# Optimization experiments

Measured on AMD Instinct MI355X. Metric: run time of the kernel, lower is better.

The kernel has to match this reference:

```python
import jax, jax.numpy as jnp
import numpy as np

N = 50000
E = 800000
IN_CH = 128
HID = 16
HEADS = 8
OUT_CH = 64
NEG_SLOPE = 0.2


def setup_inputs() -> dict:
    key = jax.random.key(0)
    ks = jax.random.split(key, 16)
    x = jax.random.normal(ks[0], (N, IN_CH), dtype=jnp.float32)
    edge_index = jax.random.randint(ks[1], (2, E), 0, N, dtype=jnp.int64)
    s = 0.05
    # GATv2 layer 1: in=128 -> heads=8, out=16 (concat -> 128)
    W1l = jax.random.normal(ks[2], (IN_CH, HEADS * HID), dtype=jnp.float32) * s
    b1l = jnp.zeros((HEADS * HID,), dtype=jnp.float32)
    W1r = jax.random.normal(ks[3], (IN_CH, HEADS * HID), dtype=jnp.float32) * s
    b1r = jnp.zeros((HEADS * HID,), dtype=jnp.float32)
    att1 = jax.random.normal(ks[4], (HEADS, HID), dtype=jnp.float32) * s
    bias1 = jnp.zeros((HEADS * HID,), dtype=jnp.float32)
    # GATv2 layer 2: in=128 -> heads=1, out=64
    W2l = jax.random.normal(ks[5], (HEADS * HID, OUT_CH), dtype=jnp.float32) * s
    b2l = jnp.zeros((OUT_CH,), dtype=jnp.float32)
    W2r = jax.random.normal(ks[6], (HEADS * HID, OUT_CH), dtype=jnp.float32) * s
    b2r = jnp.zeros((OUT_CH,), dtype=jnp.float32)
    att2 = jax.random.normal(ks[7], (1, OUT_CH), dtype=jnp.float32) * s
    bias2 = jnp.zeros((OUT_CH,), dtype=jnp.float32)
    return dict(x=x, edge_index=edge_index,
                W1l=W1l, b1l=b1l, W1r=W1r, b1r=b1r, att1=att1, bias1=bias1,
                W2l=W2l, b2l=b2l, W2r=W2r, b2r=b2r, att2=att2, bias2=bias2)


def gatv2_conv(x, src, dst, Wl, bl, Wr, br, att, bias, heads, out_ch, concat):
    n = x.shape[0]
    xl = (x @ Wl + bl).reshape(n, heads, out_ch)  # source transform
    xr = (x @ Wr + br).reshape(n, heads, out_ch)  # target transform
    m = xl[src] + xr[dst]                          # [E, H, C]
    m = jnp.where(m > 0, m, NEG_SLOPE * m)         # LeakyReLU(0.2)
    alpha = jnp.einsum('ehc,hc->eh', m, att)       # [E, H]
    # segment softmax over destination nodes (every node has a self loop)
    amax = jax.ops.segment_max(alpha, dst, num_segments=n)
    ea = jnp.exp(alpha - amax[dst])
    denom = jax.ops.segment_sum(ea, dst, num_segments=n)
    w = ea / denom[dst]                            # [E, H]
    out = jax.ops.segment_sum(xl[src] * w[:, :, None], dst, num_segments=n)
    if concat:
        out = out.reshape(n, heads * out_ch)
    else:
        out = out.mean(axis=1)
    return out + bias


def reference(x, edge_index, W1l, b1l, W1r, b1r, att1, bias1,
              W2l, b2l, W2r, b2r, att2, bias2):
    n = x.shape[0]
    loops = jnp.arange(n, dtype=edge_index.dtype)
    src = jnp.concatenate([edge_index[0], loops])
    dst = jnp.concatenate([edge_index[1], loops])
    # dropout layers are identity in eval mode
    h = gatv2_conv(x, src, dst, W1l, b1l, W1r, b1r, att1, bias1,
                   heads=HEADS, out_ch=HID, concat=True)
    h = jax.nn.elu(h)
    out = gatv2_conv(h, src, dst, W2l, b2l, W2r, b2r, att2, bias2,
                     heads=1, out_ch=OUT_CH, concat=True)
    return out
```

## Files before the change

kernel.cpp:

```cpp
#include <hip/hip_runtime.h>
#include <hip/hip_bf16.h>

constexpr int N_  = 50000;
constexpr int E_  = 800000;
constexpr int ET_ = 850000;
constexpr float NEG_SLOPE = 0.2f;

constexpr int SCAN_NB = (N_ + 255) / 256;
constexpr int CSR_CAP = 1250008;
constexpr int HT      = ET_ / 8;
constexpr int HB      = (HT + 255) / 256;
constexpr int G1A     = 1563;
constexpr int G1Bb    = 1562;
constexpr int ZERO4   = (50000 + CSR_CAP) / 4;

typedef __attribute__((ext_vector_type(8))) short short8;
typedef __attribute__((ext_vector_type(4))) float f32x4;

__device__ inline float leaky(float v) { return fmaxf(v, NEG_SLOPE * v); }

__device__ inline unsigned bf16rn(float f) {
    union { float f; unsigned u; } v; v.f = f;
    return (v.u + 0x7fffu + ((v.u >> 16) & 1u)) >> 16;
}
__device__ inline float2 unpack2(unsigned u) {
    return make_float2(__uint_as_float(u << 16), __uint_as_float(u & 0xffff0000u));
}

__global__ __launch_bounds__(256) void init_kernel(
        const float* __restrict__ W1l, const float* __restrict__ W1r,
        const float* __restrict__ W2l, const float* __restrict__ W2r,
        unsigned short* __restrict__ wsw, unsigned short* __restrict__ wsw2,
        int4* __restrict__ zbase) {
    int gid = blockIdx.x * 256 + threadIdx.x;
    if (gid < ZERO4) zbase[gid] = make_int4(0, 0, 0, 0);
    if (gid < 32768) {
        int j    = gid & 7;
        int lane = (gid >> 3) & 63;
        int ks   = (gid >> 9) & 3;
        int ct   = gid >> 11;
        int k = ks * 32 + ((lane >> 4) & 3) * 8 + j;
        int c = ct * 16 + (lane & 15);
        float v = (c < 128) ? W1l[k * 128 + c] : W1r[k * 128 + (c - 128)];
        wsw[gid] = (unsigned short)bf16rn(v);
    } else if (gid < 49152) {
        int t2   = gid - 32768;
        int j    = t2 & 7;
        int lane = (t2 >> 3) & 63;
        int ks   = (t2 >> 9) & 3;
        int ct   = t2 >> 11;
        int k = ks * 32 + ((lane >> 4) & 3) * 8 + j;
        int c = ct * 16 + (lane & 15);
        float v = (c < 64) ? W2l[k * 64 + c] : W2r[k * 64 + (c - 64)];
        wsw2[t2] = (unsigned short)bf16rn(v);
    }
}

__global__ __launch_bounds__(256) void scan_partial(
        const int* __restrict__ count, int* __restrict__ bsum) {
    __shared__ int red[256];
    int t = threadIdx.x;
    int i = blockIdx.x * 256 + t;
    red[t] = (i < N_) ? ((count[i] + 7) & ~7) : 0;
    __syncthreads();
    #pragma unroll
    for (int o = 128; o > 0; o >>= 1) {
        if (t < o) red[t] += red[t + o];
        __syncthreads();
    }
    if (t == 0) bsum[blockIdx.x] = red[0];
}

__global__ __launch_bounds__(256) void scan_final2(
        const int* __restrict__ count, const int* __restrict__ bsum,
        int* __restrict__ start, int* __restrict__ cur) {
    __shared__ int top[256];
    __shared__ int buf[256];
    int t = threadIdx.x;
    top[t] = (t < SCAN_NB) ? bsum[t] : 0;
    __syncthreads();
    #pragma unroll
    for (int o = 1; o < 256; o <<= 1) {
        int add = (t >= o) ? top[t - o] : 0;
        __syncthreads();
        top[t] += add;
        __syncthreads();
    }
    int bst = (blockIdx.x == 0) ? 0 : top[blockIdx.x - 1];
    int i = blockIdx.x * 256 + t;
    int v = (i < N_) ? ((count[i] + 7) & ~7) : 0;
    buf[t] = v;
    __syncthreads();
    #pragma unroll
    for (int o = 1; o < 256; o <<= 1) {
        int add = (t >= o) ? buf[t - o] : 0;
        __syncthreads();
        buf[t] += add;
        __syncthreads();
    }
    if (i < N_) {
        int sv = bst + buf[t] - v;
        start[i] = sv;
        cur[i]   = sv;
    }
}

__global__ __launch_bounds__(256) void edge_gemm1(
        const int phase, const int nbase,
        const int* __restrict__ ei, int* __restrict__ count,
        int* __restrict__ cur, int* __restrict__ csr_src,
        const float* __restrict__ x, const unsigned short* __restrict__ wsw,
        const float* __restrict__ bl, const float* __restrict__ br,
        unsigned short* __restrict__ xlu, float* __restrict__ xr1) {
    __shared__ unsigned short lu[16][132];
    __shared__ float          lr[16][132];
    if (blockIdx.x < HB) {
        int t = blockIdx.x * 256 + threadIdx.x;
        if (t >= HT) return;
        int e8 = t * 8;
        if (phase == 0) {
            int d[8];
            if (e8 < E_) {
                int4 a = *(const int4*)(ei + E_ + e8);
                int4 b = *(const int4*)(ei + E_ + e8 + 4);
                d[0] = a.x; d[1] = a.y; d[2] = a.z; d[3] = a.w;
                d[4] = b.x; d[5] = b.y; d[6] = b.z; d[7] = b.w;
            } else {
                #pragma unroll
                for (int i = 0; i < 8; ++i) d[i] = e8 + i - E_;
            }
            #pragma unroll
            for (int i = 0; i < 8; ++i) atomicAdd(&count[d[i]], 1);
        } else {
            int s[8], d[8];
            if (e8 < E_) {
                int4 sa = *(const int4*)(ei + e8);
                int4 sb = *(const int4*)(ei + e8 + 4);
                int4 da = *(const int4*)(ei + E_ + e8);
                int4 db = *(const int4*)(ei + E_ + e8 + 4);
                s[0] = sa.x; s[1] = sa.y; s[2] = sa.z; s[3] = sa.w;
                s[4] = sb.x; s[5] = sb.y; s[6] = sb.z; s[7] = sb.w;
                d[0] = da.x; d[1] = da.y; d[2] = da.z; d[3] = da.w;
                d[4] = db.x; d[5] = db.y; d[6] = db.z; d[7] = db.w;
            } else {
                #pragma unroll
                for (int i = 0; i < 8; ++i) { s[i] = e8 + i - E_; d[i] = s[i]; }
            }
            int o[8];
            #pragma unroll
            for (int i = 0; i < 8; ++i) o[i] = atomicAdd(&cur[d[i]], 1);
            #pragma unroll
            for (int i = 0; i < 8; ++i) csr_src[o[i]] = s[i];
        }
        return;
    }
    const int blk  = blockIdx.x - HB;
    const int wave = threadIdx.x >> 6;
    const int lane = threadIdx.x & 63;
    const int n0 = nbase + blk * 16;
    const int m = lane & 15;
    const int q = (lane >> 4) & 3;
    const float* __restrict__ arow = x + (size_t)(n0 + m) * 128 + q * 8;
    short8 afrag[4];
    #pragma unroll
    for (int ks = 0; ks < 4; ++ks) {
        float4 v0 = *(const float4*)(arow + ks * 32);
        float4 v1 = *(const float4*)(arow + ks * 32 + 4);
        short8 a;
        a[0] = (short)bf16rn(v0.x); a[1] = (short)bf16rn(v0.y);
        a[2] = (short)bf16rn(v0.z); a[3] = (short)bf16rn(v0.w);
        a[4] = (short)bf16rn(v1.x); a[5] = (short)bf16rn(v1.y);
        a[6] = (short)bf16rn(v1.z); a[7] = (short)bf16rn(v1.w);
        afrag[ks] = a;
    }
    #pragma unroll
    for (int i = 0; i < 4; ++i) {
        const int ct = wave * 4 + i;
        f32x4 acc = {0.f, 0.f, 0.f, 0.f};
        #pragma unroll
        for (int ks = 0; ks < 4; ++ks) {
            short8 b = *(const short8*)(wsw + ((size_t)(ct * 4 + ks) * 64 + lane) * 8);
            acc = __builtin_amdgcn_mfma_f32_16x16x32_bf16(afrag[ks], b, acc, 0, 0, 0);
        }
        if (ct < 8) {
            const int col = ct * 16 + m;
            float bias = bl[col];
            #pragma unroll
            for (int j = 0; j < 4; ++j)
                lu[q * 4 + j][col] = (unsigned short)bf16rn(acc[j] + bias);
        } else {
            const int col = (ct - 8) * 16 + m;
            float bias = br[col];
            #pragma unroll
            for (int j = 0; j < 4; ++j)
                lr[q * 4 + j][col] = acc[j] + bias;
        }
    }
    __syncthreads();
    unsigned* __restrict__ xlu32 = (unsigned*)xlu;
    #pragma unroll
    for (int k = 0; k < 4; ++k) {
        int r = wave * 4 + k;
        unsigned w = *(const unsigned*)&lu[r][2 * lane];
        xlu32[(size_t)(n0 + r) * 64 + lane] = w;
        float2 f = make_float2(lr[r][2 * lane], lr[r][2 * lane + 1]);
        *(float2*)(xr1 + (size_t)(n0 + r) * 128 + 2 * lane) = f;
    }
}

__global__ __launch_bounds__(256) void fused1(
        const int* __restrict__ csr_src, const int* __restrict__ start,
        const int* __restrict__ count,
        const unsigned* __restrict__ xl1b, const float* __restrict__ xr1,
        const float* __restrict__ att, const float* __restrict__ bias1,
        float* __restrict__ hout) {
    int t = blockIdx.x * 256 + threadIdx.x;
    int n = __builtin_amdgcn_readfirstlane(t >> 6);
    int lane = t & 63;
    if (n >= N_) return;
    float2 xr = *(const float2*)(xr1 + (size_t)n * 128 + 2 * lane);
    float2 av = *(const float2*)(att + 2 * lane);
    int p0 = __builtin_amdgcn_readfirstlane(start[n]);
    int p1 = p0 + __builtin_amdgcn_readfirstlane(count[n]);
    float2 acc = make_float2(0.f, 0.f);
    float l = 0.f;
    for (int p = p0; p < p1; p += 8) {
        int4 ia = *(const int4*)(csr_src + p);
        int4 ib = *(const int4*)(csr_src + p + 4);
        int s0 = __builtin_amdgcn_readfirstlane(ia.x);
        int s1 = __builtin_amdgcn_readfirstlane(ia.y);
        int s2 = __builtin_amdgcn_readfirstlane(ia.z);
        int s3 = __builtin_amdgcn_readfirstlane(ia.w);
        int s4 = __builtin_amdgcn_readfirstlane(ib.x);
        int s5 = __builtin_amdgcn_readfirstlane(ib.y);
        int s6 = __builtin_amdgcn_readfirstlane(ib.z);
        int s7 = __builtin_amdgcn_readfirstlane(ib.w);
        float2 x0 = unpack2(xl1b[(size_t)s0 * 64 + lane]);
        float2 x1 = unpack2(xl1b[(size_t)s1 * 64 + lane]);
        float2 x2 = unpack2(xl1b[(size_t)s2 * 64 + lane]);
        float2 x3 = unpack2(xl1b[(size_t)s3 * 64 + lane]);
        float2 x4 = unpack2(xl1b[(size_t)s4 * 64 + lane]);
        float2 x5 = unpack2(xl1b[(size_t)s5 * 64 + lane]);
        float2 x6 = unpack2(xl1b[(size_t)s6 * 64 + lane]);
        float2 x7 = unpack2(xl1b[(size_t)s7 * 64 + lane]);
        float a0 = fmaf(leaky(x0.x + xr.x), av.x, leaky(x0.y + xr.y) * av.y);
        float a1 = fmaf(leaky(x1.x + xr.x), av.x, leaky(x1.y + xr.y) * av.y);
        float a2 = fmaf(leaky(x2.x + xr.x), av.x, leaky(x2.y + xr.y) * av.y);
        float a3 = fmaf(leaky(x3.x + xr.x), av.x, leaky(x3.y + xr.y) * av.y);
        float a4 = fmaf(leaky(x4.x + xr.x), av.x, leaky(x4.y + xr.y) * av.y);
        float a5 = fmaf(leaky(x5.x + xr.x), av.x, leaky(x5.y + xr.y) * av.y);
        float a6 = fmaf(leaky(x6.x + xr.x), av.x, leaky(x6.y + xr.y) * av.y);
        float a7 = fmaf(leaky(x7.x + xr.x), av.x, leaky(x7.y + xr.y) * av.y);
        a0 += __shfl_xor(a0, 1); a1 += __shfl_xor(a1, 1);
        a2 += __shfl_xor(a2, 1); a3 += __shfl_xor(a3, 1);
        a4 += __shfl_xor(a4, 1); a5 += __shfl_xor(a5, 1);
        a6 += __shfl_xor(a6, 1); a7 += __shfl_xor(a7, 1);
        a0 += __shfl_xor(a0, 2); a1 += __shfl_xor(a1, 2);
        a2 += __shfl_xor(a2, 2); a3 += __shfl_xor(a3, 2);
        a4 += __shfl_xor(a4, 2); a5 += __shfl_xor(a5, 2);
        a6 += __shfl_xor(a6, 2); a7 += __shfl_xor(a7, 2);
        a0 += __shfl_xor(a0, 4); a1 += __shfl_xor(a1, 4);
        a2 += __shfl_xor(a2, 4); a3 += __shfl_xor(a3, 4);
        a4 += __shfl_xor(a4, 4); a5 += __shfl_xor(a5, 4);
        a6 += __shfl_xor(a6, 4); a7 += __shfl_xor(a7, 4);
        float w0 = __expf(a0);
        float w1 = p + 1 < p1 ? __expf(a1) : 0.f;
        float w2 = p + 2 < p1 ? __expf(a2) : 0.f;
        float w3 = p + 3 < p1 ? __expf(a3) : 0.f;
        float w4 = p + 4 < p1 ? __expf(a4) : 0.f;
        float w5 = p + 5 < p1 ? __expf(a5) : 0.f;
        float w6 = p + 6 < p1 ? __expf(a6) : 0.f;
        float w7 = p + 7 < p1 ? __expf(a7) : 0.f;
        acc.x = fmaf(w0, x0.x, acc.x); acc.y = fmaf(w0, x0.y, acc.y); l += w0;
        acc.x = fmaf(w1, x1.x, acc.x); acc.y = fmaf(w1, x1.y, acc.y); l += w1;
        acc.x = fmaf(w2, x2.x, acc.x); acc.y = fmaf(w2, x2.y, acc.y); l += w2;
        acc.x = fmaf(w3, x3.x, acc.x); acc.y = fmaf(w3, x3.y, acc.y); l += w3;
        acc.x = fmaf(w4, x4.x, acc.x); acc.y = fmaf(w4, x4.y, acc.y); l += w4;
        acc.x = fmaf(w5, x5.x, acc.x); acc.y = fmaf(w5, x5.y, acc.y); l += w5;
        acc.x = fmaf(w6, x6.x, acc.x); acc.y = fmaf(w6, x6.y, acc.y); l += w6;
        acc.x = fmaf(w7, x7.x, acc.x); acc.y = fmaf(w7, x7.y, acc.y); l += w7;
    }
    float2 bv = *(const float2*)(bias1 + 2 * lane);
    float vx = acc.x / l + bv.x;
    float vy = acc.y / l + bv.y;
    float2 o;
    o.x = vx > 0.f ? vx : (__expf(vx) - 1.f);
    o.y = vy > 0.f ? vy : (__expf(vy) - 1.f);
    *(float2*)(hout + (size_t)n * 128 + 2 * lane) = o;
}

__global__ __launch_bounds__(256) void gemm2_mfma(
        const float* __restrict__ hbuf,
        const unsigned short* __restrict__ wsw2,
        const float* __restrict__ bl, const float* __restrict__ br,
        unsigned short* __restrict__ xlu2, float* __restrict__ xr2) {
    __shared__ unsigned short lu2[16][68];
    __shared__ float          lr2[16][68];
    const int wave = threadIdx.x >> 6;
    const int lane = threadIdx.x & 63;
    const int n0 = blockIdx.x * 16;
    const int m = lane & 15;
    const int q = (lane >> 4) & 3;
    const float* __restrict__ arow = hbuf + (size_t)(n0 + m) * 128 + q * 8;
    short8 afrag[4];
    #pragma unroll
    for (int ks = 0; ks < 4; ++ks) {
        float4 v0 = *(const float4*)(arow + ks * 32);
        float4 v1 = *(const float4*)(arow + ks * 32 + 4);
        short8 a;
        a[0] = (short)bf16rn(v0.x); a[1] = (short)bf16rn(v0.y);
        a[2] = (short)bf16rn(v0.z); a[3] = (short)bf16rn(v0.w);
        a[4] = (short)bf16rn(v1.x); a[5] = (short)bf16rn(v1.y);
        a[6] = (short)bf16rn(v1.z); a[7] = (short)bf16rn(v1.w);
        afrag[ks] = a;
    }
    #pragma unroll
    for (int i = 0; i < 2; ++i) {
        const int ct = wave * 2 + i;
        f32x4 acc = {0.f, 0.f, 0.f, 0.f};
        #pragma unroll
        for (int ks = 0; ks < 4; ++ks) {
            short8 b = *(const short8*)(wsw2 + ((size_t)(ct * 4 + ks) * 64 + lane) * 8);
            acc = __builtin_amdgcn_mfma_f32_16x16x32_bf16(afrag[ks], b, acc, 0, 0, 0);
        }
        if (ct < 4) {
            const int col = ct * 16 + m;
            float bias = bl[col];
            #pragma unroll
            for (int j = 0; j < 4; ++j)
                lu2[q * 4 + j][col] = (unsigned short)bf16rn(acc[j] + bias);
        } else {
            const int col = (ct - 4) * 16 + m;
            float bias = br[col];
            #pragma unroll
            for (int j = 0; j < 4; ++j)
                lr2[q * 4 + j][col] = acc[j] + bias;
        }
    }
    __syncthreads();
    unsigned* __restrict__ xlu232 = (unsigned*)xlu2;
    #pragma unroll
    for (int k = 0; k < 2; ++k) {
        int rr = wave * 4 + 2 * k + (lane >> 5);
        int c  = lane & 31;
        unsigned w = *(const unsigned*)&lu2[rr][2 * c];
        xlu232[(size_t)(n0 + rr) * 32 + c] = w;
    }
    #pragma unroll
    for (int k = 0; k < 4; ++k) {
        int r = wave * 4 + k;
        xr2[(size_t)(n0 + r) * 64 + lane] = lr2[r][lane];
    }
}

__global__ __launch_bounds__(256) void fused2(
        const int* __restrict__ csr_src, const int* __restrict__ start,
        const int* __restrict__ count,
        const unsigned* __restrict__ xl2b, const float* __restrict__ xr2,
        const float* __restrict__ att, const float* __restrict__ bias2,
        float* __restrict__ out) {
    int t = blockIdx.x * 256 + threadIdx.x;
    int n = __builtin_amdgcn_readfirstlane(t >> 6);
    int lane = t & 63;
    int half = lane >> 5;
    int lc   = lane & 31;
    if (n >= N_) return;
    float2 xr = *(const float2*)(xr2 + (size_t)n * 64 + 2 * lc);
    float2 av = *(const float2*)(att + 2 * lc);
    int p0 = __builtin_amdgcn_readfirstlane(start[n]);
    int p1 = p0 + __builtin_amdgcn_readfirstlane(count[n]);
    float2 acc = make_float2(0.f, 0.f);
    float l = 0.f;
    for (int p = p0; p < p1; p += 8) {
        int4 ia = *(const int4*)(csr_src + p);
        int4 ib = *(const int4*)(csr_src + p + 4);
        int sx[8];
        sx[0] = __builtin_amdgcn_readfirstlane(ia.x);
        sx[1] = __builtin_amdgcn_readfirstlane(ia.y);
        sx[2] = __builtin_amdgcn_readfirstlane(ia.z);
        sx[3] = __builtin_amdgcn_readfirstlane(ia.w);
        sx[4] = __builtin_amdgcn_readfirstlane(ib.x);
        sx[5] = __builtin_amdgcn_readfirstlane(ib.y);
        sx[6] = __builtin_amdgcn_readfirstlane(ib.z);
        sx[7] = __builtin_amdgcn_readfirstlane(ib.w);
        #pragma unroll
        for (int u = 0; u < 4; ++u) {
            int pe = p + 2 * u + half;
            int s  = sx[2 * u + half];
            float2 xv = unpack2(xl2b[(size_t)s * 32 + lc]);
            float a = fmaf(leaky(xv.x + xr.x), av.x, leaky(xv.y + xr.y) * av.y);
            a += __shfl_xor(a, 1);
            a += __shfl_xor(a, 2);
            a += __shfl_xor(a, 4);
            a += __shfl_xor(a, 8);
            a += __shfl_xor(a, 16);
            float w = pe < p1 ? __expf(a) : 0.f;
            acc.x = fmaf(w, xv.x, acc.x);
            acc.y = fmaf(w, xv.y, acc.y);
            l += w;
        }
    }
    acc.x += __shfl_xor(acc.x, 32);
    acc.y += __shfl_xor(acc.y, 32);
    l     += __shfl_xor(l, 32);
    if (half == 0) {
        float2 bv = *(const float2*)(bias2 + 2 * lc);
        float2 o;
        o.x = acc.x / l + bv.x;
        o.y = acc.y / l + bv.y;
        *(float2*)(out + (size_t)n * 64 + 2 * lc) = o;
    }
}

extern "C" void kernel_launch(void* const* d_in, const int* in_sizes, int n_in,
                              void* d_out, int out_size, void* d_ws, size_t ws_size,
                              hipStream_t stream) {
    (void)in_sizes; (void)n_in; (void)out_size; (void)ws_size;
    const float* x     = (const float*)d_in[0];
    const int*   ei    = (const int*)d_in[1];
    const float* W1l   = (const float*)d_in[2];
    const float* b1l   = (const float*)d_in[3];
    const float* W1r   = (const float*)d_in[4];
    const float* b1r   = (const float*)d_in[5];
    const float* att1  = (const float*)d_in[6];
    const float* bias1 = (const float*)d_in[7];
    const float* W2l   = (const float*)d_in[8];
    const float* b2l   = (const float*)d_in[9];
    const float* W2r   = (const float*)d_in[10];
    const float* b2r   = (const float*)d_in[11];
    const float* att2  = (const float*)d_in[12];
    const float* bias2 = (const float*)d_in[13];
    float* out = (float*)d_out;

    float* xr1      = (float*)d_ws;
    float* hbuf     = xr1 + 6400000;
    unsigned* xl1b  = (unsigned*)(hbuf + 6400000);
    int* count   = (int*)(xl1b + 3200000);
    int* csr_src = count + 50000;
    int* startp  = csr_src + CSR_CAP;
    int* cur     = startp + 50000;
    int* bsum    = cur + 850000;
    int* bstart  = bsum + 256;
    unsigned short* wsw2 = (unsigned short*)(bstart + 256);
    unsigned* xl2b = xl1b;
    float* xr2     = xr1;
    unsigned short* wsw = (unsigned short*)hbuf;

    init_kernel<<<(ZERO4 + 255) / 256, 256, 0, stream>>>(W1l, W1r, W2l, W2r,
                                                         wsw, wsw2, (int4*)count);
    edge_gemm1<<<HB + G1A, 256, 0, stream>>>(0, 0, ei, count, cur, csr_src,
                                             x, wsw, b1l, b1r,
                                             (unsigned short*)xl1b, xr1);
    scan_partial<<<SCAN_NB, 256, 0, stream>>>(count, bsum);
    scan_final2 <<<SCAN_NB, 256, 0, stream>>>(count, bsum, startp, cur);
    edge_gemm1<<<HB + G1Bb, 256, 0, stream>>>(1, G1A * 16, ei, count, cur, csr_src,
                                              x, wsw, b1l, b1r,
                                              (unsigned short*)xl1b, xr1);
    fused1<<<(N_ * 64 + 255) / 256, 256, 0, stream>>>(csr_src, startp, count,
                                                      xl1b, xr1, att1, bias1, hbuf);
    gemm2_mfma <<<N_ / 16, 256, 0, stream>>>(hbuf, wsw2, b2l, b2r,
                                             (unsigned short*)xl2b, xr2);
    fused2<<<(N_ * 64 + 255) / 256, 256, 0, stream>>>(csr_src, startp, count,
                                                      xl2b, xr2, att2, bias2, out);
}
```

Baseline: 296.7 us.

## Split CSR build into striped histogram with recorded offsets and scatter

The count atomics are spread over 8 sub-counters per destination node, chosen by thread lane. Each edge records the offset returned by its atomic, so a separate scatter kernel can place source ids without a second atomic pass. The GEMM blocks now stage the full weight tile in LDS and handle 64 rows each, writing outputs directly instead of going through an LDS transpose. This trades atomic contention for extra memory traffic: per-node 8-way count arrays, an offsets array, and less coalesced output stores.

```diff
diff --git a/kernel.cpp b/kernel.cpp
--- a/kernel.cpp
+++ b/kernel.cpp
@@ -7,12 +7,11 @@
 constexpr float NEG_SLOPE = 0.2f;
 
 constexpr int SCAN_NB = (N_ + 255) / 256;
-constexpr int CSR_CAP = 1250008;
+constexpr int CSR_CAP = 1250016;
 constexpr int HT      = ET_ / 8;
 constexpr int HB      = (HT + 255) / 256;
-constexpr int G1A     = 1563;
-constexpr int G1Bb    = 1562;
-constexpr int ZERO4   = (50000 + CSR_CAP) / 4;
+constexpr int GW      = (N_ + 63) / 64;
+constexpr int ZERO4   = (400000 + CSR_CAP) / 4;
 
 typedef __attribute__((ext_vector_type(8))) short short8;
 typedef __attribute__((ext_vector_type(4))) float f32x4;
@@ -56,111 +55,47 @@
     }
 }
 
-__global__ __launch_bounds__(256) void scan_partial(
-        const int* __restrict__ count, int* __restrict__ bsum) {
-    __shared__ int red[256];
-    int t = threadIdx.x;
-    int i = blockIdx.x * 256 + t;
-    red[t] = (i < N_) ? ((count[i] + 7) & ~7) : 0;
-    __syncthreads();
-    #pragma unroll
-    for (int o = 128; o > 0; o >>= 1) {
-        if (t < o) red[t] += red[t + o];
-        __syncthreads();
-    }
-    if (t == 0) bsum[blockIdx.x] = red[0];
-}
-
-__global__ __launch_bounds__(256) void scan_final2(
-        const int* __restrict__ count, const int* __restrict__ bsum,
-        int* __restrict__ start, int* __restrict__ cur) {
-    __shared__ int top[256];
-    __shared__ int buf[256];
-    int t = threadIdx.x;
-    top[t] = (t < SCAN_NB) ? bsum[t] : 0;
-    __syncthreads();
-    #pragma unroll
-    for (int o = 1; o < 256; o <<= 1) {
-        int add = (t >= o) ? top[t - o] : 0;
-        __syncthreads();
-        top[t] += add;
-        __syncthreads();
-    }
-    int bst = (blockIdx.x == 0) ? 0 : top[blockIdx.x - 1];
-    int i = blockIdx.x * 256 + t;
-    int v = (i < N_) ? ((count[i] + 7) & ~7) : 0;
-    buf[t] = v;
-    __syncthreads();
-    #pragma unroll
-    for (int o = 1; o < 256; o <<= 1) {
-        int add = (t >= o) ? buf[t - o] : 0;
-        __syncthreads();
-        buf[t] += add;
-        __syncthreads();
-    }
-    if (i < N_) {
-        int sv = bst + buf[t] - v;
-        start[i] = sv;
-        cur[i]   = sv;
-    }
-}
-
-__global__ __launch_bounds__(256) void edge_gemm1(
-        const int phase, const int nbase,
-        const int* __restrict__ ei, int* __restrict__ count,
-        int* __restrict__ cur, int* __restrict__ csr_src,
+__global__ __launch_bounds__(256) void hist_gemm1(
+        const int* __restrict__ ei, int* __restrict__ count8,
+        int* __restrict__ off,
         const float* __restrict__ x, const unsigned short* __restrict__ wsw,
         const float* __restrict__ bl, const float* __restrict__ br,
         unsigned short* __restrict__ xlu, float* __restrict__ xr1) {
-    __shared__ unsigned short lu[16][132];
-    __shared__ float          lr[16][132];
+    __shared__ short8 bsh[4096];
     if (blockIdx.x < HB) {
         int t = blockIdx.x * 256 + threadIdx.x;
         if (t >= HT) return;
+        int b  = t & 7;
         int e8 = t * 8;
-        if (phase == 0) {
-            int d[8];
-            if (e8 < E_) {
-                int4 a = *(const int4*)(ei + E_ + e8);
-                int4 b = *(const int4*)(ei + E_ + e8 + 4);
-                d[0] = a.x; d[1] = a.y; d[2] = a.z; d[3] = a.w;
-                d[4] = b.x; d[5] = b.y; d[6] = b.z; d[7] = b.w;
-            } else {
-                #pragma unroll
-                for (int i = 0; i < 8; ++i) d[i] = e8 + i - E_;
-            }
+        int d[8];
+        if (e8 < E_) {
+            int4 a = *(const int4*)(ei + E_ + e8);
+            int4 bb = *(const int4*)(ei + E_ + e8 + 4);
+            d[0] = a.x; d[1] = a.y; d[2] = a.z; d[3] = a.w;
+            d[4] = bb.x; d[5] = bb.y; d[6] = bb.z; d[7] = bb.w;
+        } else {
             #pragma unroll
-            for (int i = 0; i < 8; ++i) atomicAdd(&count[d[i]], 1);
-        } else {
-            int s[8], d[8];
-            if (e8 < E_) {
-                int4 sa = *(const int4*)(ei + e8);
-                int4 sb = *(const int4*)(ei + e8 + 4);
-                int4 da = *(const int4*)(ei + E_ + e8);
-                int4 db = *(const int4*)(ei + E_ + e8 + 4);
-                s[0] = sa.x; s[1] = sa.y; s[2] = sa.z; s[3] = sa.w;
-                s[4] = sb.x; s[5] = sb.y; s[6] = sb.z; s[7] = sb.w;
-                d[0] = da.x; d[1] = da.y; d[2] = da.z; d[3] = da.w;
-                d[4] = db.x; d[5] = db.y; d[6] = db.z; d[7] = db.w;
-            } else {
-                #pragma unroll
-                for (int i = 0; i < 8; ++i) { s[i] = e8 + i - E_; d[i] = s[i]; }
-            }
-            int o[8];
-            #pragma unroll
-            for (int i = 0; i < 8; ++i) o[i] = atomicAdd(&cur[d[i]], 1);
-            #pragma unroll
-            for (int i = 0; i < 8; ++i) csr_src[o[i]] = s[i];
+            for (int i = 0; i < 8; ++i) d[i] = e8 + i - E_;
         }
+        int o[8];
+        #pragma unroll
+        for (int i = 0; i < 8; ++i) o[i] = atomicAdd(&count8[d[i] * 8 + b], 1);
+        int4* op = (int4*)(off + e8);
+        op[0] = make_int4(o[0], o[1], o[2], o[3]);
+        op[1] = make_int4(o[4], o[5], o[6], o[7]);
         return;
     }
+    const short8* wg = (const short8*)wsw;
+    for (int i = threadIdx.x; i < 4096; i += 256) bsh[i] = wg[i];
+    __syncthreads();
     const int blk  = blockIdx.x - HB;
     const int wave = threadIdx.x >> 6;
     const int lane = threadIdx.x & 63;
-    const int n0 = nbase + blk * 16;
+    const int rbase = blk * 64 + wave * 16;
     const int m = lane & 15;
     const int q = (lane >> 4) & 3;
-    const float* __restrict__ arow = x + (size_t)(n0 + m) * 128 + q * 8;
+    int rl = rbase + m; if (rl >= N_) rl = N_ - 1;
+    const float* __restrict__ arow = x + (size_t)rl * 128 + q * 8;
     short8 afrag[4];
     #pragma unroll
     for (int ks = 0; ks < 4; ++ks) {
@@ -174,43 +109,138 @@
         afrag[ks] = a;
     }
     #pragma unroll
-    for (int i = 0; i < 4; ++i) {
-        const int ct = wave * 4 + i;
+    for (int ct = 0; ct < 16; ++ct) {
         f32x4 acc = {0.f, 0.f, 0.f, 0.f};
         #pragma unroll
-        for (int ks = 0; ks < 4; ++ks) {
-            short8 b = *(const short8*)(wsw + ((size_t)(ct * 4 + ks) * 64 + lane) * 8);
-            acc = __builtin_amdgcn_mfma_f32_16x16x32_bf16(afrag[ks], b, acc, 0, 0, 0);
-        }
+        for (int ks = 0; ks < 4; ++ks)
+            acc = __builtin_amdgcn_mfma_f32_16x16x32_bf16(
+                      afrag[ks], bsh[(ct * 4 + ks) * 64 + lane], acc, 0, 0, 0);
+        const int col = ct * 16 + m;
         if (ct < 8) {
-            const int col = ct * 16 + m;
             float bias = bl[col];
             #pragma unroll
-            for (int j = 0; j < 4; ++j)
-                lu[q * 4 + j][col] = (unsigned short)bf16rn(acc[j] + bias);
+            for (int j = 0; j < 4; ++j) {
+                int row = rbase + q * 4 + j;
+                if (row < N_)
+                    xlu[(size_t)row * 128 + col] = (unsigned short)bf16rn(acc[j] + bias);
+            }
         } else {
-            const int col = (ct - 8) * 16 + m;
-            float bias = br[col];
+            float bias = br[col - 128];
             #pragma unroll
-            for (int j = 0; j < 4; ++j)
-                lr[q * 4 + j][col] = acc[j] + bias;
+            for (int j = 0; j < 4; ++j) {
+                int row = rbase + q * 4 + j;
+                if (row < N_)
+                    xr1[(size_t)row * 128 + (col - 128)] = acc[j] + bias;
+            }
         }
     }
+}
+
+__global__ __launch_bounds__(256) void scan_partial(
+        const int* __restrict__ count8, int* __restrict__ bsum) {
+    __shared__ int red[256];
+    int t = threadIdx.x;
+    int i = blockIdx.x * 256 + t;
+    int v = 0;
+    if (i < N_) {
+        int4 c0 = *(const int4*)(count8 + i * 8);
+        int4 c1 = *(const int4*)(count8 + i * 8 + 4);
+        int s = c0.x + c0.y + c0.z + c0.w + c1.x + c1.y + c1.z + c1.w;
+        v = (s + 7) & ~7;
+    }
+    red[t] = v;
     __syncthreads();
-    unsigned* __restrict__ xlu32 = (unsigned*)xlu;
-    #pragma unroll
-    for (int k = 0; k < 4; ++k) {
-        int r = wave * 4 + k;
-        unsigned w = *(const unsigned*)&lu[r][2 * lane];
-        xlu32[(size_t)(n0 + r) * 64 + lane] = w;
-        float2 f = make_float2(lr[r][2 * lane], lr[r][2 * lane + 1]);
-        *(float2*)(xr1 + (size_t)(n0 + r) * 128 + 2 * lane) = f;
-    }
+    #pragma unroll
+    for (int o = 128; o > 0; o >>= 1) {
+        if (t < o) red[t] += red[t + o];
+        __syncthreads();
+    }
+    if (t == 0) bsum[blockIdx.x] = red[0];
+}
+
+__global__ __launch_bounds__(256) void scan_final2(
+        const int* __restrict__ count8, const int* __restrict__ bsum,
+        int* __restrict__ start, int* __restrict__ cnt, int* __restrict__ cur8) {
+    __shared__ int top[256];
+    __shared__ int buf[256];
+    int t = threadIdx.x;
+    top[t] = (t < SCAN_NB) ? bsum[t] : 0;
+    __syncthreads();
+    #pragma unroll
+    for (int o = 1; o < 256; o <<= 1) {
+        int add = (t >= o) ? top[t - o] : 0;
+        __syncthreads();
+        top[t] += add;
+        __syncthreads();
+    }
+    int bst = (blockIdx.x == 0) ? 0 : top[blockIdx.x - 1];
+    int i = blockIdx.x * 256 + t;
+    int4 c0 = make_int4(0,0,0,0), c1 = make_int4(0,0,0,0);
+    int sum = 0;
+    if (i < N_) {
+        c0 = *(const int4*)(count8 + i * 8);
+        c1 = *(const int4*)(count8 + i * 8 + 4);
+        sum = c0.x + c0.y + c0.z + c0.w + c1.x + c1.y + c1.z + c1.w;
+    }
+    int v = (sum + 7) & ~7;
+    buf[t] = v;
+    __syncthreads();
+    #pragma unroll
+    for (int o = 1; o < 256; o <<= 1) {
+        int add = (t >= o) ? buf[t - o] : 0;
+        __syncthreads();
+        buf[t] += add;
+        __syncthreads();
+    }
+    if (i < N_) {
+        int sv = bst + buf[t] - v;
+        start[i] = sv;
+        cnt[i]   = sum;
+        int pr = sv;
+        int4 w0, w1;
+        w0.x = pr; pr += c0.x; w0.y = pr; pr += c0.y;
+        w0.z = pr; pr += c0.z; w0.w = pr; pr += c0.w;
+        w1.x = pr; pr += c1.x; w1.y = pr; pr += c1.y;
+        w1.z = pr; pr += c1.z; w1.w = pr;
+        *(int4*)(cur8 + i * 8)     = w0;
+        *(int4*)(cur8 + i * 8 + 4) = w1;
+    }
+}
+
+__global__ __launch_bounds__(256) void scatter_kernel(
+        const int* __restrict__ ei, const int* __restrict__ cur8,
+        const int* __restrict__ off, int* __restrict__ csr_src) {
+    int t = blockIdx.x * 256 + threadIdx.x;
+    if (t >= HT) return;
+    int b  = t & 7;
+    int e8 = t * 8;
+    int4 o0 = *(const int4*)(off + e8);
+    int4 o1 = *(const int4*)(off + e8 + 4);
+    int o[8] = {o0.x, o0.y, o0.z, o0.w, o1.x, o1.y, o1.z, o1.w};
+    int s[8], d[8];
+    if (e8 < E_) {
+        int4 sa = *(const int4*)(ei + e8);
+        int4 sb = *(const int4*)(ei + e8 + 4);
+        int4 da = *(const int4*)(ei + E_ + e8);
+        int4 db = *(const int4*)(ei + E_ + e8 + 4);
+        s[0] = sa.x; s[1] = sa.y; s[2] = sa.z; s[3] = sa.w;
+        s[4] = sb.x; s[5] = sb.y; s[6] = sb.z; s[7] = sb.w;
+        d[0] = da.x; d[1] = da.y; d[2] = da.z; d[3] = da.w;
+        d[4] = db.x; d[5] = db.y; d[6] = db.z; d[7] = db.w;
+    } else {
+        #pragma unroll
+        for (int i = 0; i < 8; ++i) { s[i] = e8 + i - E_; d[i] = s[i]; }
+    }
+    int base[8];
+    #pragma unroll
+    for (int i = 0; i < 8; ++i) base[i] = cur8[d[i] * 8 + b];
+    #pragma unroll
+    for (int i = 0; i < 8; ++i) csr_src[base[i] + o[i]] = s[i];
 }
 
 __global__ __launch_bounds__(256) void fused1(
         const int* __restrict__ csr_src, const int* __restrict__ start,
-        const int* __restrict__ count,
+        const int* __restrict__ cnt,
         const unsigned* __restrict__ xl1b, const float* __restrict__ xr1,
         const float* __restrict__ att, const float* __restrict__ bias1,
         float* __restrict__ hout) {
@@ -221,7 +251,7 @@
     float2 xr = *(const float2*)(xr1 + (size_t)n * 128 + 2 * lane);
     float2 av = *(const float2*)(att + 2 * lane);
     int p0 = __builtin_amdgcn_readfirstlane(start[n]);
-    int p1 = p0 + __builtin_amdgcn_readfirstlane(count[n]);
+    int p1 = p0 + __builtin_amdgcn_readfirstlane(cnt[n]);
     float2 acc = make_float2(0.f, 0.f);
     float l = 0.f;
     for (int p = p0; p < p1; p += 8) {
@@ -294,14 +324,17 @@
         const unsigned short* __restrict__ wsw2,
         const float* __restrict__ bl, const float* __restrict__ br,
         unsigned short* __restrict__ xlu2, float* __restrict__ xr2) {
-    __shared__ unsigned short lu2[16][68];
-    __shared__ float          lr2[16][68];
+    __shared__ short8 bsh[2048];
+    const short8* wg = (const short8*)wsw2;
+    for (int i = threadIdx.x; i < 2048; i += 256) bsh[i] = wg[i];
+    __syncthreads();
     const int wave = threadIdx.x >> 6;
     const int lane = threadIdx.x & 63;
-    const int n0 = blockIdx.x * 16;
+    const int rbase = blockIdx.x * 64 + wave * 16;
     const int m = lane & 15;
     const int q = (lane >> 4) & 3;
-    const float* __restrict__ arow = hbuf + (size_t)(n0 + m) * 128 + q * 8;
+    int rl = rbase + m; if (rl >= N_) rl = N_ - 1;
+    const float* __restrict__ arow = hbuf + (size_t)rl * 128 + q * 8;
     short8 afrag[4];
     #pragma unroll
     for (int ks = 0; ks < 4; ++ks) {
@@ -315,47 +348,36 @@
         afrag[ks] = a;
     }
     #pragma unroll
-    for (int i = 0; i < 2; ++i) {
-        const int ct = wave * 2 + i;
+    for (int ct = 0; ct < 8; ++ct) {
         f32x4 acc = {0.f, 0.f, 0.f, 0.f};
         #pragma unroll
-        for (int ks = 0; ks < 4; ++ks) {
-            short8 b = *(const short8*)(wsw2 + ((size_t)(ct * 4 + ks) * 64 + lane) * 8);
-            acc = __builtin_amdgcn_mfma_f32_16x16x32_bf16(afrag[ks], b, acc, 0, 0, 0);
-        }
+        for (int ks = 0; ks < 4; ++ks)
+            acc = __builtin_amdgcn_mfma_f32_16x16x32_bf16(
+                      afrag[ks], bsh[(ct * 4 + ks) * 64 + lane], acc, 0, 0, 0);
+        const int col = ct * 16 + m;
         if (ct < 4) {
-            const int col = ct * 16 + m;
             float bias = bl[col];
             #pragma unroll
-            for (int j = 0; j < 4; ++j)
-                lu2[q * 4 + j][col] = (unsigned short)bf16rn(acc[j] + bias);
+            for (int j = 0; j < 4; ++j) {
+                int row = rbase + q * 4 + j;
+                if (row < N_)
+                    xlu2[(size_t)row * 64 + col] = (unsigned short)bf16rn(acc[j] + bias);
+            }
         } else {
-            const int col = (ct - 4) * 16 + m;
-            float bias = br[col];
+            float bias = br[col - 64];
             #pragma unroll
-            for (int j = 0; j < 4; ++j)
-                lr2[q * 4 + j][col] = acc[j] + bias;
+            for (int j = 0; j < 4; ++j) {
+                int row = rbase + q * 4 + j;
+                if (row < N_)
+                    xr2[(size_t)row * 64 + (col - 64)] = acc[j] + bias;
+            }
         }
-    }
-    __syncthreads();
-    unsigned* __restrict__ xlu232 = (unsigned*)xlu2;
-    #pragma unroll
-    for (int k = 0; k < 2; ++k) {
-        int rr = wave * 4 + 2 * k + (lane >> 5);
-        int c  = lane & 31;
-        unsigned w = *(const unsigned*)&lu2[rr][2 * c];
-        xlu232[(size_t)(n0 + rr) * 32 + c] = w;
-    }
-    #pragma unroll
-    for (int k = 0; k < 4; ++k) {
-        int r = wave * 4 + k;
-        xr2[(size_t)(n0 + r) * 64 + lane] = lr2[r][lane];
     }
 }
 
 __global__ __launch_bounds__(256) void fused2(
         const int* __restrict__ csr_src, const int* __restrict__ start,
-        const int* __restrict__ count,
+        const int* __restrict__ cnt,
         const unsigned* __restrict__ xl2b, const float* __restrict__ xr2,
         const float* __restrict__ att, const float* __restrict__ bias2,
         float* __restrict__ out) {
@@ -368,7 +390,7 @@
     float2 xr = *(const float2*)(xr2 + (size_t)n * 64 + 2 * lc);
     float2 av = *(const float2*)(att + 2 * lc);
     int p0 = __builtin_amdgcn_readfirstlane(start[n]);
-    int p1 = p0 + __builtin_amdgcn_readfirstlane(count[n]);
+    int p1 = p0 + __builtin_amdgcn_readfirstlane(cnt[n]);
     float2 acc = make_float2(0.f, 0.f);
     float l = 0.f;
     for (int p = p0; p < p1; p += 8) {
@@ -435,31 +457,29 @@
     float* xr1      = (float*)d_ws;
     float* hbuf     = xr1 + 6400000;
     unsigned* xl1b  = (unsigned*)(hbuf + 6400000);
-    int* count   = (int*)(xl1b + 3200000);
-    int* csr_src = count + 50000;
-    int* startp  = csr_src + CSR_CAP;
-    int* cur     = startp + 50000;
-    int* bsum    = cur + 850000;
-    int* bstart  = bsum + 256;
-    unsigned short* wsw2 = (unsigned short*)(bstart + 256);
+    int* count8  = (int*)(xl1b + 3200000);
+    int* csr_src = count8 + 400000;
+    int* cur8    = csr_src + CSR_CAP;
+    int* startp  = cur8 + 400000;
+    int* cnt     = startp + 50000;
+    int* off     = cnt + 50000;
+    int* bsum    = off + 850000;
+    unsigned short* wsw2 = (unsigned short*)(bsum + 256);
     unsigned* xl2b = xl1b;
     float* xr2     = xr1;
     unsigned short* wsw = (unsigned short*)hbuf;
 
     init_kernel<<<(ZERO4 + 255) / 256, 256, 0, stream>>>(W1l, W1r, W2l, W2r,
-                                                         wsw, wsw2, (int4*)count);
-    edge_gemm1<<<HB + G1A, 256, 0, stream>>>(0, 0, ei, count, cur, csr_src,
-                                             x, wsw, b1l, b1r,
-                                             (unsigned short*)xl1b, xr1);
-    scan_partial<<<SCAN_NB, 256, 0, stream>>>(count, bsum);
-    scan_final2 <<<SCAN_NB, 256, 0, stream>>>(count, bsum, startp, cur);
-    edge_gemm1<<<HB + G1Bb, 256, 0, stream>>>(1, G1A * 16, ei, count, cur, csr_src,
-                                              x, wsw, b1l, b1r,
-                                              (unsigned short*)xl1b, xr1);
-    fused1<<<(N_ * 64 + 255) / 256, 256, 0, stream>>>(csr_src, startp, count,
+                                                         wsw, wsw2, (int4*)count8);
+    hist_gemm1<<<HB + GW, 256, 0, stream>>>(ei, count8, off, x, wsw, b1l, b1r,
+                                            (unsigned short*)xl1b, xr1);
+    scan_partial<<<SCAN_NB, 256, 0, stream>>>(count8, bsum);
+    scan_final2 <<<SCAN_NB, 256, 0, stream>>>(count8, bsum, startp, cnt, cur8);
+    scatter_kernel<<<(HT + 255) / 256, 256, 0, stream>>>(ei, cur8, off, csr_src);
+    fused1<<<(N_ * 64 + 255) / 256, 256, 0, stream>>>(csr_src, startp, cnt,
                                                       xl1b, xr1, att1, bias1, hbuf);
-    gemm2_mfma <<<N_ / 16, 256, 0, stream>>>(hbuf, wsw2, b2l, b2r,
-                                             (unsigned short*)xl2b, xr2);
-    fused2<<<(N_ * 64 + 255) / 256, 256, 0, stream>>>(csr_src, startp, count,
+    gemm2_mfma <<<GW, 256, 0, stream>>>(hbuf, wsw2, b2l, b2r,
+                                        (unsigned short*)xl2b, xr2);
+    fused2<<<(N_ * 64 + 255) / 256, 256, 0, stream>>>(csr_src, startp, cnt,
                                                       xl2b, xr2, att2, bias2, out);
 }
```

Result: faster. 267.6 us (-9.8%).

## Build CSR via sub-binned histogram offsets and overlap fused1 halves with gemm2

Applied to the files above, without the earlier changes.

The CSR build now uses a separate histogram kernel. Each edge atomically increments one of eight sub-bins per destination and records its own offset, so the scatter pass needs no atomics. The scan computes per-sub-bin base pointers, and the scatter then runs in the same launch as the full layer-1 GEMM. Layer-1 aggregation is split into two node halves, and the gemm2 work for each half is co-scheduled in a later launch so the two stages overlap. This adds an extra offset array, eight-times-larger count storage and more kernel launches. It also reuses workspace regions for aliasing, which makes the buffer layout riskier.

```diff
diff --git a/kernel.cpp b/kernel.cpp
--- a/kernel.cpp
+++ b/kernel.cpp
@@ -7,12 +7,20 @@
 constexpr float NEG_SLOPE = 0.2f;
 
 constexpr int SCAN_NB = (N_ + 255) / 256;
-constexpr int CSR_CAP = 1250008;
+constexpr int CSR_CAP = 1250016;
+constexpr int HISTB   = (ET_ + 255) / 256;
 constexpr int HT      = ET_ / 8;
-constexpr int HB      = (HT + 255) / 256;
-constexpr int G1A     = 1563;
-constexpr int G1Bb    = 1562;
-constexpr int ZERO4   = (50000 + CSR_CAP) / 4;
+constexpr int SB      = (HT + 255) / 256;
+constexpr int G1B     = N_ / 16;
+constexpr int NA      = 25008;
+constexpr int NB      = N_ - NA;
+constexpr int F1A_B   = NA / 4;
+constexpr int G2A_B   = NA / 16;
+constexpr int F1B_B   = NB / 4;
+constexpr int G2B_B   = NB / 16;
+constexpr int ZC4     = 100000;
+constexpr int ZS4     = CSR_CAP / 4;
+constexpr int ZT4     = ZC4 + ZS4;
 
 typedef __attribute__((ext_vector_type(8))) short short8;
 typedef __attribute__((ext_vector_type(4))) float f32x4;
@@ -31,9 +39,10 @@
         const float* __restrict__ W1l, const float* __restrict__ W1r,
         const float* __restrict__ W2l, const float* __restrict__ W2r,
         unsigned short* __restrict__ wsw, unsigned short* __restrict__ wsw2,
-        int4* __restrict__ zbase) {
+        int4* __restrict__ zcount, int4* __restrict__ zcsr) {
     int gid = blockIdx.x * 256 + threadIdx.x;
-    if (gid < ZERO4) zbase[gid] = make_int4(0, 0, 0, 0);
+    if (gid < ZC4) zcount[gid] = make_int4(0, 0, 0, 0);
+    else if (gid < ZT4) zcsr[gid - ZC4] = make_int4(0, 0, 0, 0);
     if (gid < 32768) {
         int j    = gid & 7;
         int lane = (gid >> 3) & 63;
@@ -56,12 +65,28 @@
     }
 }
 
+__global__ __launch_bounds__(256) void hist_kernel(
+        const int* __restrict__ ei, int* __restrict__ count8,
+        int* __restrict__ off) {
+    int e = blockIdx.x * 256 + threadIdx.x;
+    if (e >= ET_) return;
+    int d = (e < E_) ? ei[E_ + e] : e - E_;
+    off[e] = atomicAdd(&count8[d * 8 + (e & 7)], 1);
+}
+
 __global__ __launch_bounds__(256) void scan_partial(
-        const int* __restrict__ count, int* __restrict__ bsum) {
+        const int* __restrict__ count8, int* __restrict__ bsum) {
     __shared__ int red[256];
     int t = threadIdx.x;
     int i = blockIdx.x * 256 + t;
-    red[t] = (i < N_) ? ((count[i] + 7) & ~7) : 0;
+    int v = 0;
+    if (i < N_) {
+        int4 c0 = *(const int4*)(count8 + i * 8);
+        int4 c1 = *(const int4*)(count8 + i * 8 + 4);
+        int s = c0.x + c0.y + c0.z + c0.w + c1.x + c1.y + c1.z + c1.w;
+        v = (s + 7) & ~7;
+    }
+    red[t] = v;
     __syncthreads();
     #pragma unroll
     for (int o = 128; o > 0; o >>= 1) {
@@ -72,8 +97,8 @@
 }
 
 __global__ __launch_bounds__(256) void scan_final2(
-        const int* __restrict__ count, const int* __restrict__ bsum,
-        int* __restrict__ start, int* __restrict__ cur) {
+        const int* __restrict__ count8, const int* __restrict__ bsum,
+        int* __restrict__ start, int* __restrict__ cnt, int* __restrict__ cur8) {
     __shared__ int top[256];
     __shared__ int buf[256];
     int t = threadIdx.x;
@@ -88,7 +113,14 @@
     }
     int bst = (blockIdx.x == 0) ? 0 : top[blockIdx.x - 1];
     int i = blockIdx.x * 256 + t;
-    int v = (i < N_) ? ((count[i] + 7) & ~7) : 0;
+    int4 c0 = make_int4(0,0,0,0), c1 = make_int4(0,0,0,0);
+    int sum = 0;
+    if (i < N_) {
+        c0 = *(const int4*)(count8 + i * 8);
+        c1 = *(const int4*)(count8 + i * 8 + 4);
+        sum = c0.x + c0.y + c0.z + c0.w + c1.x + c1.y + c1.z + c1.w;
+    }
+    int v = (sum + 7) & ~7;
     buf[t] = v;
     __syncthreads();
     #pragma unroll
@@ -101,63 +133,58 @@
     if (i < N_) {
         int sv = bst + buf[t] - v;
         start[i] = sv;
-        cur[i]   = sv;
-    }
-}
-
-__global__ __launch_bounds__(256) void edge_gemm1(
-        const int phase, const int nbase,
-        const int* __restrict__ ei, int* __restrict__ count,
-        int* __restrict__ cur, int* __restrict__ csr_src,
+        cnt[i]   = sum;
+        int pr = sv;
+        int4 w0, w1;
+        w0.x = pr; pr += c0.x; w0.y = pr; pr += c0.y;
+        w0.z = pr; pr += c0.z; w0.w = pr; pr += c0.w;
+        w1.x = pr; pr += c1.x; w1.y = pr; pr += c1.y;
+        w1.z = pr; pr += c1.z; w1.w = pr;
+        *(int4*)(cur8 + i * 8)     = w0;
+        *(int4*)(cur8 + i * 8 + 4) = w1;
+    }
+}
+
+__global__ __launch_bounds__(256) void scatter_gemm1(
+        const int* __restrict__ ei, const int* __restrict__ cur8,
+        const int* __restrict__ off, int* __restrict__ csr_src,
         const float* __restrict__ x, const unsigned short* __restrict__ wsw,
         const float* __restrict__ bl, const float* __restrict__ br,
         unsigned short* __restrict__ xlu, float* __restrict__ xr1) {
     __shared__ unsigned short lu[16][132];
     __shared__ float          lr[16][132];
-    if (blockIdx.x < HB) {
+    if (blockIdx.x < SB) {
         int t = blockIdx.x * 256 + threadIdx.x;
         if (t >= HT) return;
         int e8 = t * 8;
-        if (phase == 0) {
-            int d[8];
-            if (e8 < E_) {
-                int4 a = *(const int4*)(ei + E_ + e8);
-                int4 b = *(const int4*)(ei + E_ + e8 + 4);
-                d[0] = a.x; d[1] = a.y; d[2] = a.z; d[3] = a.w;
-                d[4] = b.x; d[5] = b.y; d[6] = b.z; d[7] = b.w;
-            } else {
-                #pragma unroll
-                for (int i = 0; i < 8; ++i) d[i] = e8 + i - E_;
-            }
+        int4 o0 = *(const int4*)(off + e8);
+        int4 o1 = *(const int4*)(off + e8 + 4);
+        int o[8] = {o0.x, o0.y, o0.z, o0.w, o1.x, o1.y, o1.z, o1.w};
+        int s[8], d[8];
+        if (e8 < E_) {
+            int4 sa = *(const int4*)(ei + e8);
+            int4 sb = *(const int4*)(ei + e8 + 4);
+            int4 da = *(const int4*)(ei + E_ + e8);
+            int4 db = *(const int4*)(ei + E_ + e8 + 4);
+            s[0] = sa.x; s[1] = sa.y; s[2] = sa.z; s[3] = sa.w;
+            s[4] = sb.x; s[5] = sb.y; s[6] = sb.z; s[7] = sb.w;
+            d[0] = da.x; d[1] = da.y; d[2] = da.z; d[3] = da.w;
+            d[4] = db.x; d[5] = db.y; d[6] = db.z; d[7] = db.w;
+        } else {
             #pragma unroll
-            for (int i = 0; i < 8; ++i) atomicAdd(&count[d[i]], 1);
-        } else {
-            int s[8], d[8];
-            if (e8 < E_) {
-                int4 sa = *(const int4*)(ei + e8);
-                int4 sb = *(const int4*)(ei + e8 + 4);
-                int4 da = *(const int4*)(ei + E_ + e8);
-                int4 db = *(const int4*)(ei + E_ + e8 + 4);
-                s[0] = sa.x; s[1] = sa.y; s[2] = sa.z; s[3] = sa.w;
-                s[4] = sb.x; s[5] = sb.y; s[6] = sb.z; s[7] = sb.w;
-                d[0] = da.x; d[1] = da.y; d[2] = da.z; d[3] = da.w;
-                d[4] = db.x; d[5] = db.y; d[6] = db.z; d[7] = db.w;
-            } else {
-                #pragma unroll
-                for (int i = 0; i < 8; ++i) { s[i] = e8 + i - E_; d[i] = s[i]; }
-            }
-            int o[8];
-            #pragma unroll
-            for (int i = 0; i < 8; ++i) o[i] = atomicAdd(&cur[d[i]], 1);
-            #pragma unroll
-            for (int i = 0; i < 8; ++i) csr_src[o[i]] = s[i];
-        }
+            for (int i = 0; i < 8; ++i) { s[i] = e8 + i - E_; d[i] = s[i]; }
+        }
+        int base[8];
+        #pragma unroll
+        for (int i = 0; i < 8; ++i) base[i] = cur8[d[i] * 8 + i];
+        #pragma unroll
+        for (int i = 0; i < 8; ++i) csr_src[base[i] + o[i]] = s[i];
         return;
     }
-    const int blk  = blockIdx.x - HB;
+    const int blk  = blockIdx.x - SB;
     const int wave = threadIdx.x >> 6;
     const int lane = threadIdx.x & 63;
-    const int n0 = nbase + blk * 16;
+    const int n0 = blk * 16;
     const int m = lane & 15;
     const int q = (lane >> 4) & 3;
     const float* __restrict__ arow = x + (size_t)(n0 + m) * 128 + q * 8;
@@ -208,20 +235,83 @@
     }
 }
 
-__global__ __launch_bounds__(256) void fused1(
+__global__ __launch_bounds__(256) void fused1_gemm2(
+        const int g2nb, const int g2base, const int f1base,
         const int* __restrict__ csr_src, const int* __restrict__ start,
-        const int* __restrict__ count,
+        const int* __restrict__ cnt,
         const unsigned* __restrict__ xl1b, const float* __restrict__ xr1,
         const float* __restrict__ att, const float* __restrict__ bias1,
-        float* __restrict__ hout) {
-    int t = blockIdx.x * 256 + threadIdx.x;
-    int n = __builtin_amdgcn_readfirstlane(t >> 6);
-    int lane = t & 63;
+        float* __restrict__ hout,
+        const unsigned short* __restrict__ wsw2,
+        const float* __restrict__ b2l, const float* __restrict__ b2r,
+        unsigned short* __restrict__ xlu2, float* __restrict__ xr2) {
+    __shared__ unsigned short lu2[16][68];
+    __shared__ float          lr2[16][68];
+    const int wave = threadIdx.x >> 6;
+    const int lane = threadIdx.x & 63;
+    if ((int)blockIdx.x < g2nb) {
+        const int n0 = g2base + blockIdx.x * 16;
+        const int m = lane & 15;
+        const int q = (lane >> 4) & 3;
+        const float* __restrict__ arow = hout + (size_t)(n0 + m) * 128 + q * 8;
+        short8 afrag[4];
+        #pragma unroll
+        for (int ks = 0; ks < 4; ++ks) {
+            float4 v0 = *(const float4*)(arow + ks * 32);
+            float4 v1 = *(const float4*)(arow + ks * 32 + 4);
+            short8 a;
+            a[0] = (short)bf16rn(v0.x); a[1] = (short)bf16rn(v0.y);
+            a[2] = (short)bf16rn(v0.z); a[3] = (short)bf16rn(v0.w);
+            a[4] = (short)bf16rn(v1.x); a[5] = (short)bf16rn(v1.y);
+            a[6] = (short)bf16rn(v1.z); a[7] = (short)bf16rn(v1.w);
+            afrag[ks] = a;
+        }
+        #pragma unroll
+        for (int i = 0; i < 2; ++i) {
+            const int ct = wave * 2 + i;
+            f32x4 acc = {0.f, 0.f, 0.f, 0.f};
+            #pragma unroll
+            for (int ks = 0; ks < 4; ++ks) {
+                short8 b = *(const short8*)(wsw2 + ((size_t)(ct * 4 + ks) * 64 + lane) * 8);
+                acc = __builtin_amdgcn_mfma_f32_16x16x32_bf16(afrag[ks], b, acc, 0, 0, 0);
+            }
+            if (ct < 4) {
+                const int col = ct * 16 + m;
+                float bias = b2l[col];
+                #pragma unroll
+                for (int j = 0; j < 4; ++j)
+                    lu2[q * 4 + j][col] = (unsigned short)bf16rn(acc[j] + bias);
+            } else {
+                const int col = (ct - 4) * 16 + m;
+                float bias = b2r[col];
+                #pragma unroll
+                for (int j = 0; j < 4; ++j)
+                    lr2[q * 4 + j][col] = acc[j] + bias;
+            }
+        }
+        __syncthreads();
+        unsigned* __restrict__ xlu232 = (unsigned*)xlu2;
+        #pragma unroll
+        for (int k = 0; k < 2; ++k) {
+            int rr = wave * 4 + 2 * k + (lane >> 5);
+            int c  = lane & 31;
+            unsigned w = *(const unsigned*)&lu2[rr][2 * c];
+            xlu232[(size_t)(n0 + rr) * 32 + c] = w;
+        }
+        #pragma unroll
+        for (int k = 0; k < 4; ++k) {
+            int r = wave * 4 + k;
+            xr2[(size_t)(n0 + r) * 64 + lane] = lr2[r][lane];
+        }
+        return;
+    }
+    int n = __builtin_amdgcn_readfirstlane(
+                f1base + ((int)blockIdx.x - g2nb) * 4 + wave);
     if (n >= N_) return;
     float2 xr = *(const float2*)(xr1 + (size_t)n * 128 + 2 * lane);
     float2 av = *(const float2*)(att + 2 * lane);
     int p0 = __builtin_amdgcn_readfirstlane(start[n]);
-    int p1 = p0 + __builtin_amdgcn_readfirstlane(count[n]);
+    int p1 = p0 + __builtin_amdgcn_readfirstlane(cnt[n]);
     float2 acc = make_float2(0.f, 0.f);
     float l = 0.f;
     for (int p = p0; p < p1; p += 8) {
@@ -289,73 +379,9 @@
     *(float2*)(hout + (size_t)n * 128 + 2 * lane) = o;
 }
 
-__global__ __launch_bounds__(256) void gemm2_mfma(
-        const float* __restrict__ hbuf,
-        const unsigned short* __restrict__ wsw2,
-        const float* __restrict__ bl, const float* __restrict__ br,
-        unsigned short* __restrict__ xlu2, float* __restrict__ xr2) {
-    __shared__ unsigned short lu2[16][68];
-    __shared__ float          lr2[16][68];
-    const int wave = threadIdx.x >> 6;
-    const int lane = threadIdx.x & 63;
-    const int n0 = blockIdx.x * 16;
-    const int m = lane & 15;
-    const int q = (lane >> 4) & 3;
-    const float* __restrict__ arow = hbuf + (size_t)(n0 + m) * 128 + q * 8;
-    short8 afrag[4];
-    #pragma unroll
-    for (int ks = 0; ks < 4; ++ks) {
-        float4 v0 = *(const float4*)(arow + ks * 32);
-        float4 v1 = *(const float4*)(arow + ks * 32 + 4);
-        short8 a;
-        a[0] = (short)bf16rn(v0.x); a[1] = (short)bf16rn(v0.y);
-        a[2] = (short)bf16rn(v0.z); a[3] = (short)bf16rn(v0.w);
-        a[4] = (short)bf16rn(v1.x); a[5] = (short)bf16rn(v1.y);
-        a[6] = (short)bf16rn(v1.z); a[7] = (short)bf16rn(v1.w);
-        afrag[ks] = a;
-    }
-    #pragma unroll
-    for (int i = 0; i < 2; ++i) {
-        const int ct = wave * 2 + i;
-        f32x4 acc = {0.f, 0.f, 0.f, 0.f};
-        #pragma unroll
-        for (int ks = 0; ks < 4; ++ks) {
-            short8 b = *(const short8*)(wsw2 + ((size_t)(ct * 4 + ks) * 64 + lane) * 8);
-            acc = __builtin_amdgcn_mfma_f32_16x16x32_bf16(afrag[ks], b, acc, 0, 0, 0);
-        }
-        if (ct < 4) {
-            const int col = ct * 16 + m;
-            float bias = bl[col];
-            #pragma unroll
-            for (int j = 0; j < 4; ++j)
-                lu2[q * 4 + j][col] = (unsigned short)bf16rn(acc[j] + bias);
-        } else {
-            const int col = (ct - 4) * 16 + m;
-            float bias = br[col];
-            #pragma unroll
-            for (int j = 0; j < 4; ++j)
-                lr2[q * 4 + j][col] = acc[j] + bias;
-        }
-    }
-    __syncthreads();
-    unsigned* __restrict__ xlu232 = (unsigned*)xlu2;
-    #pragma unroll
-    for (int k = 0; k < 2; ++k) {
-        int rr = wave * 4 + 2 * k + (lane >> 5);
-        int c  = lane & 31;
-        unsigned w = *(const unsigned*)&lu2[rr][2 * c];
-        xlu232[(size_t)(n0 + rr) * 32 + c] = w;
-    }
-    #pragma unroll
-    for (int k = 0; k < 4; ++k) {
-        int r = wave * 4 + k;
-        xr2[(size_t)(n0 + r) * 64 + lane] = lr2[r][lane];
-    }
-}
-
 __global__ __launch_bounds__(256) void fused2(
         const int* __restrict__ csr_src, const int* __restrict__ start,
-        const int* __restrict__ count,
+        const int* __restrict__ cnt,
         const unsigned* __restrict__ xl2b, const float* __restrict__ xr2,
         const float* __restrict__ att, const float* __restrict__ bias2,
         float* __restrict__ out) {
@@ -368,7 +394,7 @@
     float2 xr = *(const float2*)(xr2 + (size_t)n * 64 + 2 * lc);
     float2 av = *(const float2*)(att + 2 * lc);
     int p0 = __builtin_amdgcn_readfirstlane(start[n]);
-    int p1 = p0 + __builtin_amdgcn_readfirstlane(count[n]);
+    int p1 = p0 + __builtin_amdgcn_readfirstlane(cnt[n]);
     float2 acc = make_float2(0.f, 0.f);
     float l = 0.f;
     for (int p = p0; p < p1; p += 8) {
@@ -435,31 +461,39 @@
     float* xr1      = (float*)d_ws;
     float* hbuf     = xr1 + 6400000;
     unsigned* xl1b  = (unsigned*)(hbuf + 6400000);
-    int* count   = (int*)(xl1b + 3200000);
-    int* csr_src = count + 50000;
+    int* count8  = (int*)(xl1b + 3200000);
+    int* off     = count8 + 400000;
+    int* cur8    = off + 850000;
+    int* csr_src = cur8 + 400000;
     int* startp  = csr_src + CSR_CAP;
-    int* cur     = startp + 50000;
-    int* bsum    = cur + 850000;
-    int* bstart  = bsum + 256;
-    unsigned short* wsw2 = (unsigned short*)(bstart + 256);
-    unsigned* xl2b = xl1b;
+    int* cnt     = startp + 50000;
+    int* bsum    = cnt + 50000;
+    unsigned short* wsw2 = (unsigned short*)(bsum + 256);
+    unsigned* xl2b = (unsigned*)count8;
     float* xr2     = xr1;
     unsigned short* wsw = (unsigned short*)hbuf;
 
-    init_kernel<<<(ZERO4 + 255) / 256, 256, 0, stream>>>(W1l, W1r, W2l, W2r,
-                                                         wsw, wsw2, (int4*)count);
-    edge_gemm1<<<HB + G1A, 256, 0, stream>>>(0, 0, ei, count, cur, csr_src,
-                                             x, wsw, b1l, b1r,
-                                             (unsigned short*)xl1b, xr1);
-    scan_partial<<<SCAN_NB, 256, 0, stream>>>(count, bsum);
-    scan_final2 <<<SCAN_NB, 256, 0, stream>>>(count, bsum, startp, cur);
-    edge_gemm1<<<HB + G1Bb, 256, 0, stream>>>(1, G1A * 16, ei, count, cur, csr_src,
-                                              x, wsw, b1l, b1r,
-                                              (unsigned short*)xl1b, xr1);
-    fused1<<<(N_ * 64 + 255) / 256, 256, 0, stream>>>(csr_src, startp, count,
-                                                      xl1b, xr1, att1, bias1, hbuf);
-    gemm2_mfma <<<N_ / 16, 256, 0, stream>>>(hbuf, wsw2, b2l, b2r,
-                                             (unsigned short*)xl2b, xr2);
-    fused2<<<(N_ * 64 + 255) / 256, 256, 0, stream>>>(csr_src, startp, count,
+    init_kernel<<<(ZT4 + 255) / 256, 256, 0, stream>>>(W1l, W1r, W2l, W2r,
+                                                       wsw, wsw2,
+                                                       (int4*)count8, (int4*)csr_src);
+    hist_kernel<<<HISTB, 256, 0, stream>>>(ei, count8, off);
+    scan_partial<<<SCAN_NB, 256, 0, stream>>>(count8, bsum);
+    scan_final2 <<<SCAN_NB, 256, 0, stream>>>(count8, bsum, startp, cnt, cur8);
+    scatter_gemm1<<<SB + G1B, 256, 0, stream>>>(ei, cur8, off, csr_src,
+                                                x, wsw, b1l, b1r,
+                                                (unsigned short*)xl1b, xr1);
+    fused1_gemm2<<<F1A_B, 256, 0, stream>>>(0, 0, 0,
+                                            csr_src, startp, cnt, xl1b, xr1,
+                                            att1, bias1, hbuf, wsw2, b2l, b2r,
+                                            (unsigned short*)xl2b, xr2);
+    fused1_gemm2<<<G2A_B + F1B_B, 256, 0, stream>>>(G2A_B, 0, NA,
+                                            csr_src, startp, cnt, xl1b, xr1,
+                                            att1, bias1, hbuf, wsw2, b2l, b2r,
+                                            (unsigned short*)xl2b, xr2);
+    fused1_gemm2<<<G2B_B, 256, 0, stream>>>(G2B_B, NA, 0,
+                                            csr_src, startp, cnt, xl1b, xr1,
+                                            att1, bias1, hbuf, wsw2, b2l, b2r,
+                                            (unsigned short*)xl2b, xr2);
+    fused2<<<(N_ * 64 + 255) / 256, 256, 0, stream>>>(csr_src, startp, cnt,
                                                       xl2b, xr2, att2, bias2, out);
 }
```

Result: faster. 272.9 us (-8.0%).
